# Kernel tuning notes

Hardware: AMD Instinct MI355X
Metric: run time of the kernel (lower is better)

The kernel has to match this reference:

```python
import jax, jax.numpy as jnp
import numpy as np

NUM_KNOTS = 256
DEGREE = 3
NUM_BASIS = NUM_KNOTS - DEGREE - 1  # 252
N = 1_048_576


def setup_inputs() -> dict:
    key = jax.random.key(0)
    # evaluation points in [-pi, pi), shape [N, 1] like the torch module
    x = jax.random.uniform(key, (N, 1), jnp.float32, -np.pi, np.pi)
    # knot vector: constant buffer from __init__
    knots = jnp.linspace(-np.pi, np.pi, NUM_KNOTS, dtype=jnp.float32)
    return {"x": x, "knots": knots}


def reference(x, knots):
    """Cox-de Boor B-spline basis, computed bottom-up (dynamic programming).

    Mathematically identical to the naive recursion in the torch module:
    same indicator base case ([knots[j], knots[j+1])) and same denominator>0
    guards, but each level is computed once and fully vectorized over N and j.
    """
    xs = x[:, 0]  # [N]
    # degree-0 basis: indicator of half-open knot interval -> [N, K-1]
    B = ((knots[:-1] <= xs[:, None]) & (xs[:, None] < knots[1:])).astype(jnp.float32)
    for k in range(1, DEGREE + 1):
        m = NUM_KNOTS - 1 - k  # number of basis functions at level k
        d1 = knots[k:k + m] - knots[:m]          # knots[j+k]   - knots[j]
        d2 = knots[k + 1:k + 1 + m] - knots[1:1 + m]  # knots[j+k+1] - knots[j+1]
        w1 = jnp.where(d1 > 0, (xs[:, None] - knots[:m]) / jnp.where(d1 > 0, d1, 1.0), 0.0)
        w2 = jnp.where(d2 > 0, (knots[k + 1:k + 1 + m] - xs[:, None]) / jnp.where(d2 > 0, d2, 1.0), 0.0)
        B = w1 * B[:, :m] + w2 * B[:, 1:1 + m]
    # level DEGREE already has exactly NUM_BASIS columns
    return B[:, :NUM_BASIS]
```

## Files before the change

### kernel.cpp

```cpp
#include <hip/hip_runtime.h>


constexpr int NUM_KNOTS = 256;
constexpr int NUM_BASIS = 252;
constexpr int CHUNKS    = 63;
constexpr int ROWS      = 256;

typedef float f4 __attribute__((ext_vector_type(4)));

__global__ __launch_bounds__(256) void bspline_kernel(
    const float* __restrict__ X, const float* __restrict__ knots,
    float* __restrict__ out, int n)
{
    __shared__ f4  s_cb[ROWS];
    __shared__ int s_j0[ROWS];

    const int tid  = threadIdx.x;
    const int base = blockIdx.x * ROWS;
    const int row  = base + tid;

    {
        float x = X[min(row, n - 1)];
        float k0   = knots[0];
        float kend = knots[NUM_KNOTS - 1];
        float inv_h = (float)(NUM_KNOTS - 1) / (kend - k0);

        int j0 = (int)floorf((x - k0) * inv_h);
        j0 = min(max(j0, 0), NUM_KNOTS - 2);
        while (j0 > 0 && x < knots[j0]) --j0;
        while (j0 < NUM_KNOTS - 2 && x >= knots[j0 + 1]) ++j0;

        float cb[4] = {1.0f, 0.0f, 0.0f, 0.0f};
        #pragma unroll
        for (int k = 1; k <= 3; ++k) {
            #pragma unroll
            for (int i = 3; i >= 0; --i) {
                if (i > k) continue;
                int j = j0 - k + i;
                float plo = (i >= 1)     ? cb[i - 1] : 0.0f;
                float phi = (i <= k - 1) ? cb[i]     : 0.0f;
                float val = 0.0f;
                if (j >= 0 && j <= NUM_KNOTS - 2 - k) {
                    float kj  = knots[j];
                    float kj1 = knots[j + 1];
                    float kjk = knots[j + k];
                    float kk1 = knots[j + k + 1];
                    val = (x - kj) / (kjk - kj) * plo
                        + (kk1 - x) / (kk1 - kj1) * phi;
                }
                cb[i] = val;
            }
        }
        f4 cv; cv.x = cb[0]; cv.y = cb[1]; cv.z = cb[2]; cv.w = cb[3];
        s_cb[tid] = cv;
        s_j0[tid] = j0;
    }
    __syncthreads();

    int r = tid / CHUNKS;
    int c = tid - r * CHUNKS;
    f4* dst = (f4*)(out + (size_t)base * NUM_BASIS) + tid;
    const bool full = (base + ROWS <= n);

    #pragma unroll 2
    for (int it = 0; it < CHUNKS; ++it) {
        f4  cv = s_cb[r];
        int j0 = s_j0[r];
        int d  = c * 4 - (j0 - 3);
        f4 v;
        #pragma unroll
        for (int rr = 0; rr < 4; ++rr) {
            int e = d + rr;
            float val = 0.0f;
            val = (e == 0) ? cv.x : val;
            val = (e == 1) ? cv.y : val;
            val = (e == 2) ? cv.z : val;
            val = (e == 3) ? cv.w : val;
            v[rr] = val;
        }
        if (full || base + r < n)
            __builtin_nontemporal_store(v, dst);
        dst += 256;
        r += 4; c += 4;
        if (c >= CHUNKS) { c -= CHUNKS; ++r; }
    }
}

extern "C" void kernel_launch(void* const* d_in, const int* in_sizes, int n_in,
                              void* d_out, int out_size, void* d_ws, size_t ws_size,
                              hipStream_t stream) {
    const float* x     = (const float*)d_in[0];
    const float* knots = (const float*)d_in[1];
    float* out = (float*)d_out;
    int n = in_sizes[0];
    int grid = (n + ROWS - 1) / ROWS;
    bspline_kernel<<<grid, 256, 0, stream>>>(x, knots, out, n);
}
```

Baseline: 213.2 us.

## Precompute aligned chunk vectors per row and stage knots in shared memory

Stages the knot vector in shared memory so the interval search and the Cox-de Boor loop stop reading it from global memory. Each row's four basis values are pre-shifted into two aligned float4 chunks (lo/hi) plus their chunk indices, so the store loop does two compares and selects instead of a per-element index comparison chain. It also swaps the nontemporal stores for ordinary stores and changes the unroll factor from 2 to 3. The kernel is dominated by output writes, so the compute savings may matter little, and dropping the nontemporal hint may change cache behaviour for the large write stream.

```diff
diff --git a/kernel.cpp b/kernel.cpp
--- a/kernel.cpp
+++ b/kernel.cpp
@@ -12,23 +12,28 @@
     const float* __restrict__ X, const float* __restrict__ knots,
     float* __restrict__ out, int n)
 {
-    __shared__ f4  s_cb[ROWS];
-    __shared__ int s_j0[ROWS];
+    __shared__ float s_knots[NUM_KNOTS];
+    __shared__ f4   s_vlo[ROWS];
+    __shared__ f4   s_vhi[ROWS];
+    __shared__ int2 s_cc[ROWS];
 
     const int tid  = threadIdx.x;
     const int base = blockIdx.x * ROWS;
     const int row  = base + tid;
 
+    s_knots[tid] = knots[tid];
+    __syncthreads();
+
     {
-        float x = X[min(row, n - 1)];
-        float k0   = knots[0];
-        float kend = knots[NUM_KNOTS - 1];
+        float x    = X[min(row, n - 1)];
+        float k0   = s_knots[0];
+        float kend = s_knots[NUM_KNOTS - 1];
         float inv_h = (float)(NUM_KNOTS - 1) / (kend - k0);
 
         int j0 = (int)floorf((x - k0) * inv_h);
         j0 = min(max(j0, 0), NUM_KNOTS - 2);
-        while (j0 > 0 && x < knots[j0]) --j0;
-        while (j0 < NUM_KNOTS - 2 && x >= knots[j0 + 1]) ++j0;
+        while (j0 > 0 && x < s_knots[j0]) --j0;
+        while (j0 < NUM_KNOTS - 2 && x >= s_knots[j0 + 1]) ++j0;
 
         float cb[4] = {1.0f, 0.0f, 0.0f, 0.0f};
         #pragma unroll
@@ -41,19 +46,31 @@
                 float phi = (i <= k - 1) ? cb[i]     : 0.0f;
                 float val = 0.0f;
                 if (j >= 0 && j <= NUM_KNOTS - 2 - k) {
-                    float kj  = knots[j];
-                    float kj1 = knots[j + 1];
-                    float kjk = knots[j + k];
-                    float kk1 = knots[j + k + 1];
+                    float kj  = s_knots[j];
+                    float kj1 = s_knots[j + 1];
+                    float kjk = s_knots[j + k];
+                    float kk1 = s_knots[j + k + 1];
                     val = (x - kj) / (kjk - kj) * plo
                         + (kk1 - x) / (kk1 - kj1) * phi;
                 }
                 cb[i] = val;
             }
         }
-        f4 cv; cv.x = cb[0]; cv.y = cb[1]; cv.z = cb[2]; cv.w = cb[3];
-        s_cb[tid] = cv;
-        s_j0[tid] = j0;
+
+        int s = j0 - 3;
+        int a = s & 3;
+        int clo = s >> 2;
+        float lo0=cb[0], lo1=cb[1], lo2=cb[2], lo3=cb[3];
+        float hi0=0.f, hi1=0.f, hi2=0.f, hi3=0.f;
+        if (a & 2) { hi3=hi1; hi2=hi0; hi1=lo3; hi0=lo2;
+                     lo3=lo1; lo2=lo0; lo1=0.f; lo0=0.f; }
+        if (a & 1) { hi3=hi2; hi2=hi1; hi1=hi0; hi0=lo3;
+                     lo3=lo2; lo2=lo1; lo1=lo0; lo0=0.f; }
+        f4 vlo; vlo.x=lo0; vlo.y=lo1; vlo.z=lo2; vlo.w=lo3;
+        f4 vhi; vhi.x=hi0; vhi.y=hi1; vhi.z=hi2; vhi.w=hi3;
+        s_vlo[tid] = vlo;
+        s_vhi[tid] = vhi;
+        s_cc[tid]  = make_int2(clo, clo + 1);
     }
     __syncthreads();
 
@@ -62,24 +79,19 @@
     f4* dst = (f4*)(out + (size_t)base * NUM_BASIS) + tid;
     const bool full = (base + ROWS <= n);
 
-    #pragma unroll 2
+    #pragma unroll 3
     for (int it = 0; it < CHUNKS; ++it) {
-        f4  cv = s_cb[r];
-        int j0 = s_j0[r];
-        int d  = c * 4 - (j0 - 3);
+        f4   vlo = s_vlo[r];
+        f4   vhi = s_vhi[r];
+        int2 cc  = s_cc[r];
+        bool blo = (c == cc.x);
+        bool bhi = (c == cc.y);
         f4 v;
         #pragma unroll
-        for (int rr = 0; rr < 4; ++rr) {
-            int e = d + rr;
-            float val = 0.0f;
-            val = (e == 0) ? cv.x : val;
-            val = (e == 1) ? cv.y : val;
-            val = (e == 2) ? cv.z : val;
-            val = (e == 3) ? cv.w : val;
-            v[rr] = val;
-        }
+        for (int t = 0; t < 4; ++t)
+            v[t] = blo ? vlo[t] : (bhi ? vhi[t] : 0.0f);
         if (full || base + r < n)
-            __builtin_nontemporal_store(v, dst);
+            dst[0] = v;
         dst += 256;
         r += 4; c += 4;
         if (c >= CHUNKS) { c -= CHUNKS; ++r; }
```

Measured after the change: 202.8 us. 4.9% less time.
